# Kernel optimization log

Hardware: AMD Instinct MI355X
Metric: run time of the kernel (lower is better)

## Reference

```python
import jax, jax.numpy as jnp
import numpy as np

# Architecture constants (from init_kwargs / ActionConfig)
R = 4          # vae_time_compression_ratio
WS = 2         # windows_size
PAD_T = R * WS # preprocessor left-padding
HID = 512      # action hidden_size
KD_IN = 16     # keyboard_dim_in (movement feature dim)
C_IMG = 3072   # img_hidden_size
KH = 1024      # keyboard_hidden_dim
NH = 16        # heads_num
HD = 64        # keyboard_head_dim
EPS = 1e-6


def setup_inputs() -> dict:
    key = jax.random.key(0)
    ks = jax.random.split(key, 8)
    B, T, Hs, Ws, NF = 1, 3, 44, 80, 81
    S = Hs * Ws

    def w(k, shape, s=0.02):
        return jax.random.normal(k, shape, jnp.float32) * s

    return {
        "x": jax.random.normal(ks[0], (B, T * S, C_IMG), jnp.float32),
        "condition": jax.random.normal(ks[1], (B, NF, KD_IN), jnp.float32),
        "me_w1": w(ks[2], (KD_IN, HID)), "me_b1": jnp.zeros((HID,), jnp.float32),
        "me_w2": w(ks[3], (HID, HID)), "me_b2": jnp.zeros((HID,), jnp.float32),
        "q_w": w(ks[4], (C_IMG, KH)), "q_b": jnp.zeros((KH,), jnp.float32),
        "kv_w": w(ks[5], (HID * WS * R, 2 * KH)), "kv_b": jnp.zeros((2 * KH,), jnp.float32),
        "qn_w": jnp.ones((HD,), jnp.float32), "kn_w": jnp.ones((HD,), jnp.float32),
        "out_w": w(ks[6], (KH, C_IMG)), "out_b": jnp.zeros((C_IMG,), jnp.float32),
        "H": Hs, "W": Ws, "T": T, "num_frame_per_block": T,
    }


def _rmsnorm(x, w):
    return x * jax.lax.rsqrt(jnp.mean(x * x, axis=-1, keepdims=True) + EPS) * w


def _preprocess(condition, me_w1, me_b1, me_w2, me_b2, num_frame_per_block):
    # MovementPreprocessor.forward with is_causal=True
    B, NF, _ = condition.shape
    pad = jnp.broadcast_to(condition[:, :1, :], (B, PAD_T, condition.shape[-1]))
    cp = jnp.concatenate([pad, condition], axis=1)            # [B, PAD_T+NF, KD_IN]
    emb = jax.nn.silu(cp @ me_w1 + me_b1) @ me_w2 + me_b2     # [B, PAD_T+NF, HID]
    n_feats = (NF - 1) // R + 1
    start = R * (n_feats - num_frame_per_block - WS) + PAD_T  # python int (static)
    emb = emb[:, start:, :]
    # vectorized replacement of the python-loop window slicing+stack
    win = jnp.arange(num_frame_per_block)[:, None] * R + jnp.arange(WS * R)[None, :]
    gm = emb[:, win, :]                                       # [B, L, WS*R, HID]
    return gm.reshape(B, num_frame_per_block, WS * R * HID)   # [B, L, 4096]


def reference(x, condition, me_w1, me_b1, me_w2, me_b2, q_w, q_b, kv_w, kv_b,
              qn_w, kn_w, out_w, out_b, H, W, T, num_frame_per_block):
    B = x.shape[0]
    S = H * W
    L = num_frame_per_block

    mf = _preprocess(condition, me_w1, me_b1, me_w2, me_b2, L)  # [B, L, HID*WS*R]

    # q: [B, T*S, C_IMG] -> [B, S, T, h, d]
    q = (x @ q_w + q_b).reshape(B, T, S, NH, HD).transpose(0, 2, 1, 3, 4)

    # k, v: [B, L, h, d] (NOT expanded over S; broadcast inside attention instead)
    kv = (mf @ kv_w + kv_b).reshape(B, L, 2, NH, HD)
    k, v = kv[:, :, 0], kv[:, :, 1]

    q = _rmsnorm(q, qn_w)
    k = _rmsnorm(k, kn_w)

    scale = 1.0 / np.sqrt(HD).astype(np.float32)
    scores = jnp.einsum('bsthd,blhd->bshtl', q, k) * scale      # [B,S,h,T,L]
    attn = jax.nn.softmax(scores, axis=-1)
    o = jnp.einsum('bshtl,blhd->bsthd', attn, v)                # [B,S,T,h,d]

    # '(B S) T H D -> B (T S) (H D)'
    o = o.transpose(0, 2, 1, 3, 4).reshape(B, T * S, NH * HD)
    return x + (o @ out_w + out_b)
```

## Files before the change

### kernel.cpp

```cpp
#include <hip/hip_runtime.h>

#define TOK  10560
#define CIMG 3072
#define KHD  1024

typedef unsigned short ushort_t;
typedef unsigned int u32;
using bf16x8 = __attribute__((ext_vector_type(8))) __bf16;
using f32x4  = __attribute__((ext_vector_type(4))) float;

#define GLD_LDS16(gp, lp) __builtin_amdgcn_global_load_lds( \
    (const __attribute__((address_space(1))) u32*)(gp), \
    (__attribute__((address_space(3))) u32*)(lp), 16, 0, 0)

static __device__ __forceinline__ unsigned short f2bf(float f){
  union { float f; unsigned u; } x; x.f = f;
  unsigned r = x.u + 0x7fffu + ((x.u >> 16) & 1u);
  return (unsigned short)(r >> 16);
}
static __device__ __forceinline__ float wave_sum(float v){
  #pragma unroll
  for (int off = 32; off > 0; off >>= 1) v += __shfl_xor(v, off, 64);
  return v;
}

__global__ __launch_bounds__(256) void k_pre1(const float* __restrict__ cond,
    const float* __restrict__ w1, const float* __restrict__ b1,
    float* __restrict__ h1){
  __shared__ float cs[16][16];
  int t = threadIdx.x;
  if (t < 256) cs[t >> 4][t & 15] = cond[(64 + (t >> 4)) * 16 + (t & 15)];
  __syncthreads();
  #pragma unroll
  for (int i = 0; i < 4; ++i){
    int idx = blockIdx.x * 256 + t + i * 2048;
    int r = idx >> 9, c = idx & 511;
    float s = b1[c];
    #pragma unroll
    for (int j = 0; j < 16; ++j) s += cs[r][j] * w1[j * 512 + c];
    h1[idx] = s / (1.f + __expf(-s));
  }
}

__global__ __launch_bounds__(256) void k_pre2(const float* __restrict__ h1,
    const float* __restrict__ w2, const float* __restrict__ b2,
    float* __restrict__ emb){
  int idx = blockIdx.x * 256 + threadIdx.x;
  int r = idx >> 9, c = idx & 511;
  const float* hp = h1 + r * 512;
  const float* wp = w2 + c;
  float acc = b2[c];
  #pragma unroll 8
  for (int j = 0; j < 512; ++j) acc += hp[j] * wp[(size_t)j * 512];
  emb[idx] = acc;
}

__global__ __launch_bounds__(256) void k_kv(const float* __restrict__ emb,
                                            const float* __restrict__ kvw,
                                            float* __restrict__ part){
  int bl = blockIdx.x;
  int l = bl / 128, rem = bl % 128, nt = rem / 16, kc = rem % 16;
  int n = nt * 256 + threadIdx.x;
  const float* e = emb + 2048 * l + kc * 256;
  const float* w = kvw + (size_t)(kc * 256) * 2048 + n;
  float acc = 0.f;
  for (int r = 0; r < 256; ++r) acc += e[r] * w[(size_t)r * 2048];
  part[kc * 6144 + l * 2048 + n] = acc;
}

__global__ void k_knorm(const float* __restrict__ part, const float* __restrict__ kvb,
                        const float* __restrict__ knw, float* __restrict__ kn,
                        float* __restrict__ vv){
  int wid = threadIdx.x >> 6, lane = threadIdx.x & 63;
  for (int i = 0; i < 12; ++i){
    int g = wid * 12 + i;
    int l = g >> 4, h = g & 15;
    int ik = l * 2048 + h * 64 + lane;
    float kk = kvb[h * 64 + lane];
    float v  = kvb[1024 + h * 64 + lane];
    for (int p = 0; p < 16; ++p){ kk += part[p * 6144 + ik]; v += part[p * 6144 + ik + 1024]; }
    float ss = wave_sum(kk * kk);
    kn[l * 1024 + h * 64 + lane] = kk * rsqrtf(ss * (1.f/64.f) + 1e-6f) * knw[lane];
    vv[l * 1024 + h * 64 + lane] = v;
  }
}

__global__ __launch_bounds__(256) void k_tconv(const float* __restrict__ src,
                                               ushort_t* __restrict__ dst,
                                               int R, int C){
  __shared__ float tile[32][33];
  int nTr = R >> 5;
  int tr = blockIdx.x % nTr, tc = blockIdx.x / nTr;
  int r0 = tr * 32, c0 = tc * 32, t = threadIdx.x;
  #pragma unroll
  for (int i = 0; i < 4; ++i){
    int idx = t + i * 256; int r = idx >> 5, c = idx & 31;
    tile[r][c] = src[(size_t)(r0 + r) * C + c0 + c];
  }
  __syncthreads();
  #pragma unroll
  for (int i = 0; i < 4; ++i){
    int idx = t + i * 256; int rr = idx >> 5, cc = idx & 31;
    dst[(size_t)(c0 + rr) * R + r0 + cc] = f2bf(tile[cc][rr]);
  }
}

__global__ __launch_bounds__(256) void k_xconv(const float* __restrict__ x,
                                               ushort_t* __restrict__ xb, int n4){
  for (int i = blockIdx.x * 256 + threadIdx.x; i < n4; i += gridDim.x * 256){
    float4 v = ((const float4*)x)[i];
    ushort4 o;
    o.x = f2bf(v.x); o.y = f2bf(v.y); o.z = f2bf(v.z); o.w = f2bf(v.w);
    ((ushort4*)xb)[i] = o;
  }
}

__global__ __launch_bounds__(512, 2) void gemm_fused(
    const ushort_t* __restrict__ A, const ushort_t* __restrict__ Bt,
    int Mdim, int Kdim, int Ndim,
    const float* __restrict__ bias, const float* __restrict__ kn,
    const float* __restrict__ qnw, float* __restrict__ acoef){
  __shared__ __align__(16) unsigned char lds[131072];
  const int tid = threadIdx.x;
  const int lane = tid & 63, wid = tid >> 6;
  const int wm = wid >> 2, wn = wid & 3;
  const int l15 = lane & 15, kg = lane >> 4;
  const int ntiles = Ndim >> 8;

  int bid = blockIdx.x;
  const int cpx = gridDim.x >> 3;
  bid = (bid & 7) * cpx + (bid >> 3);
  const int mt = bid / ntiles, nt = bid % ntiles;
  const int mbase = mt << 8, nbase = nt << 8;

  const int sr  = tid >> 1;
  const int skh = (tid & 1) ^ ((sr >> 2) & 1);
  int arow = mbase + sr; if (arow >= Mdim) arow = Mdim - 1;
  const ushort_t* gA = A  + (size_t)arow * Kdim + skh * 8;
  const ushort_t* gB = Bt + (size_t)(nbase + sr) * Kdim + skh * 8;
  const int wofs = wid * 1024;

  auto stage = [&](int t, int c, int b){
    const int gk = t * 64 + c * 16;
    unsigned char* dst = lds + b * 65536 + c * 8192 + wofs;
    GLD_LDS16(gA + gk, dst);
    GLD_LDS16(gB + gk, dst + 32768);
  };

  const int arl = wm * 128 + l15;
  const int brl = wn * 64 + l15;
  const int kh  = ((kg & 1) ^ ((l15 >> 2) & 1)) * 16;
  const unsigned aBase = (unsigned)((kg >> 1) * 8192 + arl * 32 + kh);
  const unsigned bBase = (unsigned)(32768 + (kg >> 1) * 8192 + brl * 32 + kh);

  f32x4 acc[8][4];
  #pragma unroll
  for (int m = 0; m < 8; ++m)
    #pragma unroll
    for (int n = 0; n < 4; ++n) acc[m][n] = {0.f, 0.f, 0.f, 0.f};

  bf16x8 afr[4], bfr[4];

#define PH_READ_B(base, KSL) { _Pragma("unroll") \
    for (int n = 0; n < 4; ++n) \
      bfr[n] = *(const bf16x8*)((base) + bBase + (KSL)*16384 + n*512); }
#define PH_READ_A(base, KSL, M0) { _Pragma("unroll") \
    for (int m = 0; m < 4; ++m) \
      afr[m] = *(const bf16x8*)((base) + aBase + (KSL)*16384 + ((M0)+m)*512); }
#define PH_MFMA(R0) { __builtin_amdgcn_s_setprio(1); _Pragma("unroll") \
    for (int m = 0; m < 4; ++m){ _Pragma("unroll") \
      for (int n = 0; n < 4; ++n) \
        acc[(R0)+m][n] = __builtin_amdgcn_mfma_f32_16x16x32_bf16(afr[m], bfr[n], acc[(R0)+m][n], 0, 0, 0); } \
    __builtin_amdgcn_s_setprio(0); }

  const int T = Kdim >> 6;

  stage(0, 0, 0); stage(0, 1, 0); stage(0, 2, 0); stage(0, 3, 0);
  asm volatile("s_waitcnt vmcnt(4)" ::: "memory");
  __builtin_amdgcn_s_barrier();

  for (int t = 0; t < T - 1; ++t){
    const int b = t & 1;
    const unsigned char* base = lds + b * 65536;
    PH_READ_B(base, 0); PH_READ_A(base, 0, 0);
    stage(t + 1, 0, b ^ 1);
    __builtin_amdgcn_s_barrier();
    PH_MFMA(0);
    __builtin_amdgcn_s_barrier();
    PH_READ_A(base, 0, 4);
    stage(t + 1, 1, b ^ 1);
    asm volatile("s_waitcnt vmcnt(4)" ::: "memory");
    __builtin_amdgcn_s_barrier();
    PH_MFMA(4);
    __builtin_amdgcn_s_barrier();
    PH_READ_B(base, 1); PH_READ_A(base, 1, 0);
    stage(t + 1, 2, b ^ 1);
    __builtin_amdgcn_s_barrier();
    PH_MFMA(0);
    __builtin_amdgcn_s_barrier();
    PH_READ_A(base, 1, 4);
    stage(t + 1, 3, b ^ 1);
    asm volatile("s_waitcnt vmcnt(4)" ::: "memory");
    __builtin_amdgcn_s_barrier();
    PH_MFMA(4);
    __builtin_amdgcn_s_barrier();
  }
  {
    const unsigned char* base = lds + ((T - 1) & 1) * 65536;
    PH_READ_B(base, 0); PH_READ_A(base, 0, 0);
    __builtin_amdgcn_s_barrier();
    PH_MFMA(0);
    __builtin_amdgcn_s_barrier();
    PH_READ_A(base, 0, 4);
    asm volatile("s_waitcnt vmcnt(0)" ::: "memory");
    __builtin_amdgcn_s_barrier();
    PH_MFMA(4);
    __builtin_amdgcn_s_barrier();
    PH_READ_B(base, 1); PH_READ_A(base, 1, 0);
    PH_MFMA(0);
    PH_READ_A(base, 1, 4);
    PH_MFMA(4);
  }
#undef PH_READ_B
#undef PH_READ_A
#undef PH_MFMA

  const int hglob = nt * 4 + wn;
  float qnwv[4], qbv[4], knv0[4], knv1[4], knv2[4];
  #pragma unroll
  for (int n = 0; n < 4; ++n){
    int d = n * 16 + l15;
    qnwv[n] = qnw[d];
    qbv[n]  = bias[nbase + wn * 64 + d];
    knv0[n] = kn[hglob * 64 + d];
    knv1[n] = kn[1024 + hglob * 64 + d];
    knv2[n] = kn[2048 + hglob * 64 + d];
  }
  #pragma unroll
  for (int m = 0; m < 8; ++m){
    #pragma unroll
    for (int j = 0; j < 4; ++j){
      float q[4], ssq = 0.f;
      #pragma unroll
      for (int n = 0; n < 4; ++n){ q[n] = acc[m][n][j] + qbv[n]; ssq += q[n] * q[n]; }
      #pragma unroll
      for (int off = 1; off < 16; off <<= 1) ssq += __shfl_xor(ssq, off, 64);
      float rs = rsqrtf(ssq * (1.f/64.f) + 1e-6f);
      float s0 = 0.f, s1 = 0.f, s2 = 0.f;
      #pragma unroll
      for (int n = 0; n < 4; ++n){
        float qn = q[n] * rs * qnwv[n];
        s0 += qn * knv0[n]; s1 += qn * knv1[n]; s2 += qn * knv2[n];
      }
      #pragma unroll
      for (int off = 1; off < 16; off <<= 1){
        s0 += __shfl_xor(s0, off, 64);
        s1 += __shfl_xor(s1, off, 64);
        s2 += __shfl_xor(s2, off, 64);
      }
      s0 *= 0.125f; s1 *= 0.125f; s2 *= 0.125f;
      float mx = fmaxf(s0, fmaxf(s1, s2));
      float e0 = __expf(s0 - mx), e1 = __expf(s1 - mx), e2 = __expf(s2 - mx);
      float inv = 1.f / (e0 + e1 + e2);
      int grow = mbase + wm * 128 + m * 16 + kg * 4 + j;
      if (l15 == 0 && grow < Mdim){
        float2 a12 = {e1 * inv, e2 * inv};
        *(float2*)(acoef + (size_t)grow * 32 + hglob * 2) = a12;
      }
    }
  }
}

__global__ __launch_bounds__(512) void k_uv(const float* __restrict__ vv,
    const float* __restrict__ ow, float* __restrict__ U){
  int b = blockIdx.x;
  int i = b / 6, cc = b % 6;
  int h = i / 3, l = i % 3;
  int c = cc * 512 + threadIdx.x;
  const float* vp = vv + l * 1024 + h * 64;
  const float* wp = ow + (size_t)(h * 64) * 3072 + c;
  float acc = 0.f;
  #pragma unroll
  for (int d = 0; d < 64; ++d) acc += vp[d] * wp[(size_t)d * 3072];
  U[(size_t)i * 3072 + c] = acc;
}

__global__ __launch_bounds__(256) void k_ubase(const float* __restrict__ U,
    const float* __restrict__ ob, float* __restrict__ base, float* __restrict__ D){
  int c = blockIdx.x * 256 + threadIdx.x;
  float b = ob[c];
  #pragma unroll
  for (int h = 0; h < 16; ++h){
    float u0 = U[(size_t)(h * 3 + 0) * 3072 + c];
    float u1 = U[(size_t)(h * 3 + 1) * 3072 + c];
    float u2 = U[(size_t)(h * 3 + 2) * 3072 + c];
    b += u0;
    D[(size_t)(h * 2 + 0) * 3072 + c] = u1 - u0;
    D[(size_t)(h * 2 + 1) * 3072 + c] = u2 - u0;
  }
  base[c] = b;
}

__global__ __launch_bounds__(256) void k_rank32(const float* __restrict__ x,
    const float* __restrict__ acoef, const float* __restrict__ D,
    const float* __restrict__ base, float* __restrict__ out){
  __shared__ __align__(16) float as[120][32];
  const int tid = threadIdx.x;
  const int cc = blockIdx.x % 6, ms = blockIdx.x / 6;
  const int c = cc * 512 + tid * 2;
  const int t0 = ms * 120;

  for (int idx = tid; idx < 1920; idx += 256)
    ((float2*)as)[idx] = ((const float2*)(acoef + (size_t)t0 * 32))[idx];

  float ur0[32], ur1[32];
  #pragma unroll
  for (int i = 0; i < 32; ++i){
    float2 d2 = *(const float2*)(D + (size_t)i * 3072 + c);
    ur0[i] = d2.x; ur1[i] = d2.y;
  }
  float2 b2 = *(const float2*)(base + c);
  __syncthreads();

  #pragma unroll 2
  for (int r = 0; r < 120; ++r){
    const size_t o = (size_t)(t0 + r) * 3072 + c;
    float2 xv = *(const float2*)(x + o);
    float a0 = 0.f, a1 = 0.f;
    const f32x4* ap = (const f32x4*)as[r];
    #pragma unroll
    for (int k = 0; k < 8; ++k){
      f32x4 a4 = ap[k];
      a0 += a4[0]*ur0[4*k] + a4[1]*ur0[4*k+1] + a4[2]*ur0[4*k+2] + a4[3]*ur0[4*k+3];
      a1 += a4[0]*ur1[4*k] + a4[1]*ur1[4*k+1] + a4[2]*ur1[4*k+2] + a4[3]*ur1[4*k+3];
    }
    float2 ov = {xv.x + b2.x + a0, xv.y + b2.y + a1};
    *(float2*)(out + o) = ov;
  }
}

extern "C" void kernel_launch(void* const* d_in, const int* in_sizes, int n_in,
                              void* d_out, int out_size, void* d_ws, size_t ws_size,
                              hipStream_t stream){
  const float* x    = (const float*)d_in[0];
  const float* cond = (const float*)d_in[1];
  const float* mew1 = (const float*)d_in[2];
  const float* meb1 = (const float*)d_in[3];
  const float* mew2 = (const float*)d_in[4];
  const float* meb2 = (const float*)d_in[5];
  const float* qw   = (const float*)d_in[6];
  const float* qb   = (const float*)d_in[7];
  const float* kvw  = (const float*)d_in[8];
  const float* kvb  = (const float*)d_in[9];
  const float* qnw  = (const float*)d_in[10];
  const float* knw  = (const float*)d_in[11];
  const float* ow   = (const float*)d_in[12];
  const float* ob   = (const float*)d_in[13];

  char* ws = (char*)d_ws;
  float*    emb    = (float*)(ws + 0);
  float*    kvpart = (float*)(ws + 32768);
  float*    kn     = (float*)(ws + 425984);
  float*    vv     = (float*)(ws + 438272);
  ushort_t* qwt    = (ushort_t*)(ws + 450560);
  float*    U      = (float*)(ws + 6742016);
  float*    base   = (float*)(ws + 7331840);
  float*    Dbuf   = (float*)(ws + 7344128);
  float*    acoef  = (float*)(ws + 7737344);
  float*    h1buf  = (float*)(ws + 9089024);

  ushort_t* xb = (ushort_t*)d_out;

  k_pre1<<<8, 256, 0, stream>>>(cond, mew1, meb1, h1buf);
  k_pre2<<<32, 256, 0, stream>>>(h1buf, mew2, meb2, emb);
  k_kv<<<384, 256, 0, stream>>>(emb, kvw, kvpart);
  k_knorm<<<1, 256, 0, stream>>>(kvpart, kvb, knw, kn, vv);
  k_uv<<<288, 512, 0, stream>>>(vv, ow, U);
  k_ubase<<<12, 256, 0, stream>>>(U, ob, base, Dbuf);
  k_tconv<<<3072, 256, 0, stream>>>(qw, qwt, 3072, 1024);
  k_xconv<<<2048, 256, 0, stream>>>(x, xb, (TOK * CIMG) / 4);
  gemm_fused<<<42 * 4, 512, 0, stream>>>(xb, qwt, TOK, CIMG, KHD, qb, kn, qnw, acoef);
  k_rank32<<<88 * 6, 256, 0, stream>>>(x, acoef, Dbuf, base, (float*)d_out);
}
```

Measured before the change: 289.9 us.

## Split Q GEMM along K into three partials and move norm/softmax to separate kernel

The fused Q-projection GEMM is replaced by a split-K version that launches three times as many blocks, each covering a third of K and writing bf16 partial tiles through LDS. A new kernel sums the partials, adds bias, applies RMSNorm and computes the three-way attention softmax coefficients. This aims to fill more compute units than the previous grid, which was smaller than one wave. The cost is extra global traffic for the partials, bf16 rounding of partial sums, and an extra launch.

```diff
diff --git a/kernel.cpp b/kernel.cpp
--- a/kernel.cpp
+++ b/kernel.cpp
@@ -17,6 +17,9 @@
   union { float f; unsigned u; } x; x.f = f;
   unsigned r = x.u + 0x7fffu + ((x.u >> 16) & 1u);
   return (unsigned short)(r >> 16);
+}
+static __device__ __forceinline__ float bf2f(unsigned short u){
+  union { unsigned u; float f; } x; x.u = ((unsigned)u) << 16; return x.f;
 }
 static __device__ __forceinline__ float wave_sum(float v){
   #pragma unroll
@@ -115,29 +118,27 @@
   }
 }
 
-__global__ __launch_bounds__(512, 2) void gemm_fused(
+__global__ __launch_bounds__(512, 2) void gemm_splitk(
     const ushort_t* __restrict__ A, const ushort_t* __restrict__ Bt,
-    int Mdim, int Kdim, int Ndim,
-    const float* __restrict__ bias, const float* __restrict__ kn,
-    const float* __restrict__ qnw, float* __restrict__ acoef){
+    ushort_t* __restrict__ part){
   __shared__ __align__(16) unsigned char lds[131072];
   const int tid = threadIdx.x;
   const int lane = tid & 63, wid = tid >> 6;
   const int wm = wid >> 2, wn = wid & 3;
   const int l15 = lane & 15, kg = lane >> 4;
-  const int ntiles = Ndim >> 8;
 
   int bid = blockIdx.x;
-  const int cpx = gridDim.x >> 3;
-  bid = (bid & 7) * cpx + (bid >> 3);
-  const int mt = bid / ntiles, nt = bid % ntiles;
+  bid = (bid & 7) * 63 + (bid >> 3);
+  const int ks = bid % 3;
+  const int nt = (bid / 3) & 3;
+  const int mt = bid / 12;
   const int mbase = mt << 8, nbase = nt << 8;
 
   const int sr  = tid >> 1;
   const int skh = (tid & 1) ^ ((sr >> 2) & 1);
-  int arow = mbase + sr; if (arow >= Mdim) arow = Mdim - 1;
-  const ushort_t* gA = A  + (size_t)arow * Kdim + skh * 8;
-  const ushort_t* gB = Bt + (size_t)(nbase + sr) * Kdim + skh * 8;
+  int arow = mbase + sr; if (arow >= TOK) arow = TOK - 1;
+  const ushort_t* gA = A  + (size_t)arow * CIMG + ks * 1024 + skh * 8;
+  const ushort_t* gB = Bt + (size_t)(nbase + sr) * CIMG + ks * 1024 + skh * 8;
   const int wofs = wid * 1024;
 
   auto stage = [&](int t, int c, int b){
@@ -173,7 +174,7 @@
         acc[(R0)+m][n] = __builtin_amdgcn_mfma_f32_16x16x32_bf16(afr[m], bfr[n], acc[(R0)+m][n], 0, 0, 0); } \
     __builtin_amdgcn_s_setprio(0); }
 
-  const int T = Kdim >> 6;
+  const int T = 16;
 
   stage(0, 0, 0); stage(0, 1, 0); stage(0, 2, 0); stage(0, 3, 0);
   asm volatile("s_waitcnt vmcnt(4)" ::: "memory");
@@ -225,48 +226,69 @@
 #undef PH_READ_A
 #undef PH_MFMA
 
-  const int hglob = nt * 4 + wn;
-  float qnwv[4], qbv[4], knv0[4], knv1[4], knv2[4];
-  #pragma unroll
-  for (int n = 0; n < 4; ++n){
-    int d = n * 16 + l15;
-    qnwv[n] = qnw[d];
-    qbv[n]  = bias[nbase + wn * 64 + d];
-    knv0[n] = kn[hglob * 64 + d];
-    knv1[n] = kn[1024 + hglob * 64 + d];
-    knv2[n] = kn[2048 + hglob * 64 + d];
-  }
-  #pragma unroll
-  for (int m = 0; m < 8; ++m){
-    #pragma unroll
-    for (int j = 0; j < 4; ++j){
-      float q[4], ssq = 0.f;
-      #pragma unroll
-      for (int n = 0; n < 4; ++n){ q[n] = acc[m][n][j] + qbv[n]; ssq += q[n] * q[n]; }
-      #pragma unroll
-      for (int off = 1; off < 16; off <<= 1) ssq += __shfl_xor(ssq, off, 64);
-      float rs = rsqrtf(ssq * (1.f/64.f) + 1e-6f);
-      float s0 = 0.f, s1 = 0.f, s2 = 0.f;
+  __builtin_amdgcn_s_barrier();
+
+  ushort_t* outp = part + (size_t)ks * TOK * KHD;
+  ushort_t* cbuf = (ushort_t*)lds;
+  for (int c2 = 0; c2 < 2; ++c2){
+    if (wm == c2){
       #pragma unroll
       for (int n = 0; n < 4; ++n){
-        float qn = q[n] * rs * qnwv[n];
-        s0 += qn * knv0[n]; s1 += qn * knv1[n]; s2 += qn * knv2[n];
+        #pragma unroll
+        for (int m = 0; m < 8; ++m){
+          #pragma unroll
+          for (int j = 0; j < 4; ++j)
+            cbuf[(m * 16 + kg * 4 + j) * 256 + wn * 64 + n * 16 + l15] =
+                f2bf(acc[m][n][j]);
+        }
       }
-      #pragma unroll
-      for (int off = 1; off < 16; off <<= 1){
-        s0 += __shfl_xor(s0, off, 64);
-        s1 += __shfl_xor(s1, off, 64);
-        s2 += __shfl_xor(s2, off, 64);
-      }
-      s0 *= 0.125f; s1 *= 0.125f; s2 *= 0.125f;
-      float mx = fmaxf(s0, fmaxf(s1, s2));
-      float e0 = __expf(s0 - mx), e1 = __expf(s1 - mx), e2 = __expf(s2 - mx);
-      float inv = 1.f / (e0 + e1 + e2);
-      int grow = mbase + wm * 128 + m * 16 + kg * 4 + j;
-      if (l15 == 0 && grow < Mdim){
-        float2 a12 = {e1 * inv, e2 * inv};
-        *(float2*)(acoef + (size_t)grow * 32 + hglob * 2) = a12;
-      }
+    }
+    __syncthreads();
+    #pragma unroll
+    for (int it = 0; it < 8; ++it){
+      int r = it * 16 + (tid >> 5);
+      int cb = (tid & 31) * 8;
+      int grow = mbase + c2 * 128 + r;
+      if (grow < TOK)
+        *(uint4*)(outp + (size_t)grow * KHD + nbase + cb) =
+            *(const uint4*)(cbuf + r * 256 + cb);
+    }
+    __syncthreads();
+  }
+}
+
+__global__ __launch_bounds__(256) void k_qattn(const ushort_t* __restrict__ part,
+    const float* __restrict__ qb, const float* __restrict__ kn,
+    const float* __restrict__ qnw, float* __restrict__ acoef){
+  int wid = threadIdx.x >> 6, lane = threadIdx.x & 63;
+  int m = blockIdx.x * 4 + wid;
+  const ushort_t* p0 = part + (size_t)m * KHD;
+  const ushort_t* p1 = p0 + (size_t)TOK * KHD;
+  const ushort_t* p2 = p1 + (size_t)TOK * KHD;
+  float qwv = qnw[lane];
+  for (int h = 0; h < 16; ++h){
+    int ib = h * 64 + lane;
+    float q = bf2f(p0[ib]) + bf2f(p1[ib]) + bf2f(p2[ib]) + qb[ib];
+    float pk = q * qwv;
+    float r0 = q * q;
+    float r1 = pk * kn[ib];
+    float r2 = pk * kn[1024 + ib];
+    float r3 = pk * kn[2048 + ib];
+    #pragma unroll
+    for (int off = 32; off > 0; off >>= 1){
+      r0 += __shfl_xor(r0, off, 64);
+      r1 += __shfl_xor(r1, off, 64);
+      r2 += __shfl_xor(r2, off, 64);
+      r3 += __shfl_xor(r3, off, 64);
+    }
+    float rs = rsqrtf(r0 * (1.f/64.f) + 1e-6f) * 0.125f;
+    float s0 = r1 * rs, s1 = r2 * rs, s2 = r3 * rs;
+    float mx = fmaxf(s0, fmaxf(s1, s2));
+    float e0 = __expf(s0 - mx), e1 = __expf(s1 - mx), e2 = __expf(s2 - mx);
+    float inv = 1.f / (e0 + e1 + e2);
+    if (lane == 0){
+      float2 a12 = {e1 * inv, e2 * inv};
+      *(float2*)(acoef + (size_t)m * 32 + h * 2) = a12;
     }
   }
 }
@@ -369,7 +391,8 @@
   float*    acoef  = (float*)(ws + 7737344);
   float*    h1buf  = (float*)(ws + 9089024);
 
-  ushort_t* xb = (ushort_t*)d_out;
+  ushort_t* xb    = (ushort_t*)d_out;
+  ushort_t* qpart = xb + (size_t)TOK * CIMG;
 
   k_pre1<<<8, 256, 0, stream>>>(cond, mew1, meb1, h1buf);
   k_pre2<<<32, 256, 0, stream>>>(h1buf, mew2, meb2, emb);
@@ -379,6 +402,7 @@
   k_ubase<<<12, 256, 0, stream>>>(U, ob, base, Dbuf);
   k_tconv<<<3072, 256, 0, stream>>>(qw, qwt, 3072, 1024);
   k_xconv<<<2048, 256, 0, stream>>>(x, xb, (TOK * CIMG) / 4);
-  gemm_fused<<<42 * 4, 512, 0, stream>>>(xb, qwt, TOK, CIMG, KHD, qb, kn, qnw, acoef);
+  gemm_splitk<<<504, 512, 0, stream>>>(xb, qwt, qpart);
+  k_qattn<<<2640, 256, 0, stream>>>(qpart, qb, kn, qnw, acoef);
   k_rank32<<<88 * 6, 256, 0, stream>>>(x, acoef, Dbuf, base, (float*)d_out);
 }
```

New measurement: 334.7 us. 15.4% more time.
